# Performance work log

Measured on AMD Instinct MI355X. Metric: run time of the kernel, lower is better.

Reference implementation:

```python
import jax, jax.numpy as jnp
import numpy as np

ADC_F_BITS = 4
BIT_SCALE = 0.05
# clamp upper bound: 2^(7-f) - 1/2^f
CLAMP_MAX = 2.0 ** (7 - ADC_F_BITS) - 1.0 / 2.0 ** ADC_F_BITS  # 7.9375
N_LEVELS = 127  # 7-bit ADC characteristic


def setup_inputs() -> dict:
    key = jax.random.key(0)
    kx, kc = jax.random.split(key)
    # conv-feature-map-like activations; scale so a good fraction lies in [0, CLAMP_MAX]
    x = jax.random.normal(kx, (128, 128, 56, 56), dtype=jnp.float32) * 2.0
    # monotone ADC threshold characteristic spanning the clamp range
    adc_char = jnp.sort(
        jax.random.uniform(kc, (N_LEVELS,), dtype=jnp.float32) * CLAMP_MAX
    )
    return {"x": x, "adc_char": adc_char}


def reference(x, adc_char):
    # activation = clamp(x, 0, 2^(7-f) - 1/2^f)
    a = jnp.clip(x, 0.0, CLAMP_MAX)
    # quant_op_int = sum(a[..., None] >= adc_char, axis=-1)
    # adc_char is sorted, so this equals the count of thresholds <= a,
    # i.e. searchsorted(side='right') -- avoids the [*, 127] bool intermediate.
    q = jnp.searchsorted(adc_char, a, side="right").astype(jnp.float32)
    # op = bit_scale * quant_op_int / 2^f
    return BIT_SCALE * (q / 2.0 ** ADC_F_BITS)
```

## Files before the change

kernel.cpp:

```cpp
#include <hip/hip_runtime.h>
#include <math.h>


#define N_LEVELS 127
#define CLAMP_MAX 7.9375f
#define OUT_SCALE 0.003125f

struct TreeT {
    float T63;
    float T31, T95;
    float T15, T47, T79, T111;
    float Q0, Q1, Q2, Q3, Q4, Q5, Q6, Q7;
};

__device__ __forceinline__ float adc_eval(const float* __restrict__ my,
                                          const TreeT& t, float x) {
    float a = fminf(fmaxf(x, 0.0f), CLAMP_MAX);

    bool m0 = (t.T63 <= a);
    float s1 = m0 ? t.T95 : t.T31;
    bool m1 = (s1 <= a);
    float u0 = m0 ? t.T79  : t.T15;
    float u1 = m0 ? t.T111 : t.T47;
    float s2 = m1 ? u1 : u0;
    bool m2 = (s2 <= a);
    float x0 = m2 ? t.Q1 : t.Q0;
    float x1 = m2 ? t.Q3 : t.Q2;
    float x2 = m2 ? t.Q5 : t.Q4;
    float x3 = m2 ? t.Q7 : t.Q6;
    float y0 = m1 ? x1 : x0;
    float y1 = m1 ? x3 : x2;
    float s3 = m0 ? y1 : y0;
    bool m3 = (s3 <= a);
    int cnt = (m0 ? 64 : 0) + (m1 ? 32 : 0) + (m2 ? 16 : 0) + (m3 ? 8 : 0);

    if (my[(cnt + 3) << 5] <= a) cnt += 4;
    if (my[(cnt + 1) << 5] <= a) cnt += 2;
    if (my[(cnt + 0) << 5] <= a) cnt += 1;

    return OUT_SCALE * (float)cnt;
}

__global__ __launch_bounds__(256) void ADCActivation_55465207660703_kernel(
        const float* __restrict__ x,
        const float* __restrict__ adc_char,
        float* __restrict__ out,
        int n4, int rem) {
    __shared__ float lut[N_LEVELS * 32];

    const int tid = threadIdx.x;
    for (int i = tid; i < N_LEVELS * 32; i += 256) lut[i] = adc_char[i >> 5];
    __syncthreads();

    TreeT t;
    t.T63 = adc_char[63];
    t.T31 = adc_char[31];  t.T95  = adc_char[95];
    t.T15 = adc_char[15];  t.T47  = adc_char[47];
    t.T79 = adc_char[79];  t.T111 = adc_char[111];
    t.Q0 = adc_char[7];    t.Q1 = adc_char[23];
    t.Q2 = adc_char[39];   t.Q3 = adc_char[55];
    t.Q4 = adc_char[71];   t.Q5 = adc_char[87];
    t.Q6 = adc_char[103];  t.Q7 = adc_char[119];

    const float* my = lut + (tid & 31);

    const float4* __restrict__ x4 = (const float4*)x;
    float4* __restrict__ o4 = (float4*)out;

    const int stride = gridDim.x * 512;
    for (int i0 = blockIdx.x * 512 + tid; i0 < n4; i0 += stride) {
        const int i1 = i0 + 256;
        const bool p1 = i1 < n4;
        float4 v0 = x4[i0];
        float4 v1 = make_float4(0.f, 0.f, 0.f, 0.f);
        if (p1) v1 = x4[i1];

        float4 r0, r1;
        r0.x = adc_eval(my, t, v0.x);
        r0.y = adc_eval(my, t, v0.y);
        r0.z = adc_eval(my, t, v0.z);
        r0.w = adc_eval(my, t, v0.w);
        r1.x = adc_eval(my, t, v1.x);
        r1.y = adc_eval(my, t, v1.y);
        r1.z = adc_eval(my, t, v1.z);
        r1.w = adc_eval(my, t, v1.w);

        o4[i0] = r0;
        if (p1) o4[i1] = r1;
    }

    if (blockIdx.x == 0 && tid < rem) {
        int e = n4 * 4 + tid;
        out[e] = adc_eval(my, t, x[e]);
    }
}

extern "C" void kernel_launch(void* const* d_in, const int* in_sizes, int n_in,
                              void* d_out, int out_size, void* d_ws, size_t ws_size,
                              hipStream_t stream) {
    const float* x        = (const float*)d_in[0];
    const float* adc_char = (const float*)d_in[1];
    float* out            = (float*)d_out;

    const int n   = in_sizes[0];
    const int n4  = n >> 2;
    const int rem = n & 3;

    int blocks = (n4 + 511) / 512;
    if (blocks > 2048) blocks = 2048;
    if (blocks < 1) blocks = 1;

    ADCActivation_55465207660703_kernel<<<blocks, 256, 0, stream>>>(x, adc_char, out, n4, rem);
}
```

Baseline: 86.04 us.

## Add specialized contiguous-chunk kernel with software-prefetched loads and nontemporal stores

Adds a fast-path kernel used when the element count divides evenly into 1792 blocks of 1024 float4s per iteration. Each block walks a contiguous chunk, issuing the next iteration's four vector loads before computing the current ones (register double-buffering), and writes results with nontemporal stores to avoid polluting cache. This aims to hide memory latency better than the strided grid loop, at the cost of more registers and a shape-specific dispatch. The generic kernel is kept as a fallback.

```diff
diff --git a/kernel.cpp b/kernel.cpp
--- a/kernel.cpp
+++ b/kernel.cpp
@@ -5,6 +5,8 @@
 #define N_LEVELS 127
 #define CLAMP_MAX 7.9375f
 #define OUT_SCALE 0.003125f
+
+typedef float f32x4 __attribute__((ext_vector_type(4)));
 
 struct TreeT {
     float T63;
@@ -41,17 +43,13 @@
     return OUT_SCALE * (float)cnt;
 }
 
-__global__ __launch_bounds__(256) void ADCActivation_55465207660703_kernel(
-        const float* __restrict__ x,
-        const float* __restrict__ adc_char,
-        float* __restrict__ out,
-        int n4, int rem) {
-    __shared__ float lut[N_LEVELS * 32];
+__device__ __forceinline__ void lut_fill(float* __restrict__ lut,
+                                         const float* __restrict__ adc_char,
+                                         int tid) {
+    for (int i = tid; i < N_LEVELS * 32; i += 256) lut[i] = adc_char[i >> 5];
+}
 
-    const int tid = threadIdx.x;
-    for (int i = tid; i < N_LEVELS * 32; i += 256) lut[i] = adc_char[i >> 5];
-    __syncthreads();
-
+__device__ __forceinline__ TreeT tree_load(const float* __restrict__ adc_char) {
     TreeT t;
     t.T63 = adc_char[63];
     t.T31 = adc_char[31];  t.T95  = adc_char[95];
@@ -61,34 +59,86 @@
     t.Q2 = adc_char[39];   t.Q3 = adc_char[55];
     t.Q4 = adc_char[71];   t.Q5 = adc_char[87];
     t.Q6 = adc_char[103];  t.Q7 = adc_char[119];
+    return t;
+}
 
+__global__ __launch_bounds__(256) void adc_main_kernel(
+        const float* __restrict__ x,
+        float* __restrict__ out,
+        const float* __restrict__ adc_char,
+        int K) {
+    __shared__ float lut[N_LEVELS * 32];
+    const int tid = threadIdx.x;
+    lut_fill(lut, adc_char, tid);
+    __syncthreads();
+    const TreeT t = tree_load(adc_char);
     const float* my = lut + (tid & 31);
 
-    const float4* __restrict__ x4 = (const float4*)x;
-    float4* __restrict__ o4 = (float4*)out;
+    const f32x4* __restrict__ x4 = (const f32x4*)x;
+    f32x4* __restrict__ o4 = (f32x4*)out;
+
+    int base = blockIdx.x * (K << 10) + tid;
+
+    f32x4 v0 = x4[base], v1 = x4[base + 256], v2 = x4[base + 512], v3 = x4[base + 768];
+
+    #define BODY(B)                                                         \
+    {                                                                       \
+        f32x4 r0, r1, r2, r3;                                               \
+        r0.x = adc_eval(my, t, v0.x); r0.y = adc_eval(my, t, v0.y);         \
+        r0.z = adc_eval(my, t, v0.z); r0.w = adc_eval(my, t, v0.w);         \
+        r1.x = adc_eval(my, t, v1.x); r1.y = adc_eval(my, t, v1.y);         \
+        r1.z = adc_eval(my, t, v1.z); r1.w = adc_eval(my, t, v1.w);         \
+        r2.x = adc_eval(my, t, v2.x); r2.y = adc_eval(my, t, v2.y);         \
+        r2.z = adc_eval(my, t, v2.z); r2.w = adc_eval(my, t, v2.w);         \
+        r3.x = adc_eval(my, t, v3.x); r3.y = adc_eval(my, t, v3.y);         \
+        r3.z = adc_eval(my, t, v3.z); r3.w = adc_eval(my, t, v3.w);         \
+        __builtin_nontemporal_store(r0, &o4[(B)]);                          \
+        __builtin_nontemporal_store(r1, &o4[(B) + 256]);                    \
+        __builtin_nontemporal_store(r2, &o4[(B) + 512]);                    \
+        __builtin_nontemporal_store(r3, &o4[(B) + 768]);                    \
+    }
+
+    for (int k = 0; k < K - 1; ++k) {
+        const int nb = base + 1024;
+        f32x4 w0 = x4[nb], w1 = x4[nb + 256], w2 = x4[nb + 512], w3 = x4[nb + 768];
+        BODY(base)
+        v0 = w0; v1 = w1; v2 = w2; v3 = w3;
+        base = nb;
+    }
+    BODY(base)
+    #undef BODY
+}
+
+__global__ __launch_bounds__(256) void adc_generic_kernel(
+        const float* __restrict__ x,
+        const float* __restrict__ adc_char,
+        float* __restrict__ out,
+        int n4, int rem) {
+    __shared__ float lut[N_LEVELS * 32];
+    const int tid = threadIdx.x;
+    lut_fill(lut, adc_char, tid);
+    __syncthreads();
+    const TreeT t = tree_load(adc_char);
+    const float* my = lut + (tid & 31);
+
+    const f32x4* __restrict__ x4 = (const f32x4*)x;
+    f32x4* __restrict__ o4 = (f32x4*)out;
 
     const int stride = gridDim.x * 512;
     for (int i0 = blockIdx.x * 512 + tid; i0 < n4; i0 += stride) {
         const int i1 = i0 + 256;
         const bool p1 = i1 < n4;
-        float4 v0 = x4[i0];
-        float4 v1 = make_float4(0.f, 0.f, 0.f, 0.f);
+        f32x4 v0 = x4[i0];
+        f32x4 v1 = {0.f, 0.f, 0.f, 0.f};
         if (p1) v1 = x4[i1];
-
-        float4 r0, r1;
-        r0.x = adc_eval(my, t, v0.x);
-        r0.y = adc_eval(my, t, v0.y);
-        r0.z = adc_eval(my, t, v0.z);
-        r0.w = adc_eval(my, t, v0.w);
-        r1.x = adc_eval(my, t, v1.x);
-        r1.y = adc_eval(my, t, v1.y);
-        r1.z = adc_eval(my, t, v1.z);
-        r1.w = adc_eval(my, t, v1.w);
-
+        f32x4 r0, r1;
+        r0.x = adc_eval(my, t, v0.x); r0.y = adc_eval(my, t, v0.y);
+        r0.z = adc_eval(my, t, v0.z); r0.w = adc_eval(my, t, v0.w);
+        r1.x = adc_eval(my, t, v1.x); r1.y = adc_eval(my, t, v1.y);
+        r1.z = adc_eval(my, t, v1.z); r1.w = adc_eval(my, t, v1.w);
         o4[i0] = r0;
         if (p1) o4[i1] = r1;
     }
-
     if (blockIdx.x == 0 && tid < rem) {
         int e = n4 * 4 + tid;
         out[e] = adc_eval(my, t, x[e]);
@@ -102,13 +152,17 @@
     const float* adc_char = (const float*)d_in[1];
     float* out            = (float*)d_out;
 
-    const int n   = in_sizes[0];
-    const int n4  = n >> 2;
-    const int rem = n & 3;
+    const int n  = in_sizes[0];
+    const int n4 = n >> 2;
 
-    int blocks = (n4 + 511) / 512;
-    if (blocks > 2048) blocks = 2048;
-    if (blocks < 1) blocks = 1;
-
-    ADCActivation_55465207660703_kernel<<<blocks, 256, 0, stream>>>(x, adc_char, out, n4, rem);
+    if ((n & 3) == 0 && n4 > 0 && (n4 % (1792 * 1024)) == 0) {
+        const int K = n4 / (1792 * 1024);
+        adc_main_kernel<<<1792, 256, 0, stream>>>(x, out, adc_char, K);
+    } else {
+        const int rem = n & 3;
+        int gb = (n4 + 511) / 512;
+        if (gb > 2048) gb = 2048;
+        if (gb < 1) gb = 1;
+        adc_generic_kernel<<<gb, 256, 0, stream>>>(x, adc_char, out, n4, rem);
+    }
 }
```

After: 70.59 us (median of 2 runs). -18.0%, faster.
